# Kernel tuning notes

Hardware: AMD Instinct MI355X
Metric: run time of the kernel (lower is better)

Reference implementation:

```python
import jax, jax.numpy as jnp
import numpy as np

C_Z = 128
C_S = 1024
C_S_OUT = 1024
B, L = 1, 1024


def setup_inputs() -> dict:
    key = jax.random.key(0)
    ks = jax.random.split(key, 8)
    s_z = jax.random.normal(ks[0], (B, L, L, C_Z), dtype=jnp.float32)
    s_s_in = jax.random.normal(ks[1], (B, L, C_S), dtype=jnp.float32)
    pair_mask = jnp.ones((B, L, L), dtype=jnp.float32)
    scale = 0.02
    return {
        "s_z": s_z,
        "s_s_in": s_s_in,
        "pair_mask": pair_mask,
        "ln_g": jnp.ones((C_Z,), jnp.float32),
        "ln_b": jnp.zeros((C_Z,), jnp.float32),
        "w1": jax.random.normal(ks[2], (C_Z, C_Z), jnp.float32) * scale,
        "b1": jnp.zeros((C_Z,), jnp.float32),
        "w2": jax.random.normal(ks[3], (C_Z, C_Z), jnp.float32) * scale,
        "b2": jnp.zeros((C_Z,), jnp.float32),
        "wc": jax.random.normal(ks[4], (C_S_OUT, 2 * C_Z + C_S), jnp.float32) * scale,
        "bc": jnp.zeros((C_S_OUT,), jnp.float32),
    }


def _layernorm(x, g, b, eps=1e-5):
    mu = jnp.mean(x, axis=-1, keepdims=True)
    var = jnp.mean(jnp.square(x - mu), axis=-1, keepdims=True)
    return (x - mu) * jax.lax.rsqrt(var + eps) * g + b


def reference(s_z, s_s_in, pair_mask, ln_g, ln_b, w1, b1, w2, b2, wc, bc):
    # LayerNorm -> Linear -> ReLU -> Linear over last dim (c_z)
    z = _layernorm(s_z, ln_g, ln_b)
    z = jax.nn.relu(jnp.einsum("blmc,dc->blmd", z, w1) + b1)
    z = jnp.einsum("blmc,dc->blmd", z, w2) + b2
    z = z * pair_mask[..., None]
    # masked mean over columns (dim=2) and rows (dim=1)
    norm_c = jnp.clip(jnp.sum(pair_mask, axis=2), 1.0, None)  # (B, L)
    s_s_c = jnp.sum(z, axis=2) / norm_c[..., None]            # (B, L, c_z)
    norm_r = jnp.clip(jnp.sum(pair_mask, axis=1), 1.0, None)
    s_s_r = jnp.sum(z, axis=1) / norm_r[..., None]
    cat = jnp.concatenate([s_s_c, s_s_r, s_s_in], axis=-1)    # (B, L, 2*c_z + c_s)
    return jnp.einsum("blc,dc->bld", cat, wc) + bc            # (B, L, c_s_out)
```

## Files before the change

kernel.cpp:

```cpp
#include <hip/hip_runtime.h>
#include <hip/hip_bf16.h>


typedef short bf16x8 __attribute__((ext_vector_type(8)));
typedef float f32x16 __attribute__((ext_vector_type(16)));

static __device__ __forceinline__ short f2bf(float f) {
  unsigned u = __float_as_uint(f);
  u += 0x7fffu + ((u >> 16) & 1u);
  return (short)(u >> 16);
}
static __device__ __forceinline__ float bf2f(short s) {
  return __uint_as_float(((unsigned)(unsigned short)s) << 16);
}

__global__ __launch_bounds__(256, 2) void k_pair(
    const float* __restrict__ z, const float* __restrict__ pm,
    const float* __restrict__ lng, const float* __restrict__ lnb,
    const float* __restrict__ w1, const float* __restrict__ b1,
    float* __restrict__ g, float* __restrict__ gr)
{
  __shared__ __align__(16) char smemRaw[64 * 136 * 2];
  __shared__ float maskS[64];
  short* As   = (short*)smemRaw;
  float* red1 = (float*)smemRaw;

  const int tid  = threadIdx.x;
  const int lane = tid & 63;
  const int wv   = tid >> 6;
  const int rt   = wv >> 1;
  const int ch   = wv & 1;
  const int ln   = lane & 31;
  const int hh   = lane >> 5;
  const int l0   = blockIdx.y * 32;
  const int m0   = blockIdx.x * 32;
  const int c8   = (tid & 15) * 8;

  float lg[8], lb[8];
  #pragma unroll
  for (int j = 0; j < 8; ++j) { lg[j] = lng[c8 + j]; lb[j] = lnb[c8 + j]; }

  float b1v[2];
  #pragma unroll
  for (int cc = 0; cc < 2; ++cc) b1v[cc] = b1[(ch * 2 + cc) * 32 + ln];

  bf16x8 bF[2][8];
  #pragma unroll
  for (int cc = 0; cc < 2; ++cc) {
    const int n = (ch * 2 + cc) * 32 + ln;
    #pragma unroll
    for (int k0 = 0; k0 < 8; ++k0) {
      const float* wp = w1 + n * 128 + k0 * 16 + hh * 8;
      float4 f0 = *(const float4*)wp;
      float4 f1 = *(const float4*)(wp + 4);
      bf16x8 t;
      t[0]=f2bf(f0.x); t[1]=f2bf(f0.y); t[2]=f2bf(f0.z); t[3]=f2bf(f0.w);
      t[4]=f2bf(f1.x); t[5]=f2bf(f1.y); t[6]=f2bf(f1.z); t[7]=f2bf(f1.w);
      bF[cc][k0] = t;
    }
  }

  float grA[2][16];
  #pragma unroll
  for (int cc = 0; cc < 2; ++cc)
    #pragma unroll
    for (int i = 0; i < 16; ++i) grA[cc][i] = 0.f;

  #pragma unroll 1
  for (int b = 0; b < 16; ++b) {
    if (b) __syncthreads();
    float4 xa[4], xb[4];
    #pragma unroll
    for (int p = 0; p < 4; ++p) {
      const int r = p * 16 + (tid >> 4);
      const int l = l0 + b * 2 + (r >> 5);
      const int m = m0 + (r & 31);
      const float* src = z + ((size_t)l * 1024 + (size_t)m) * 128 + c8;
      xa[p] = *(const float4*)src;
      xb[p] = *(const float4*)(src + 4);
    }
    if (tid < 64) {
      const int l = l0 + b * 2 + (tid >> 5);
      maskS[tid] = pm[(size_t)l * 1024 + (m0 + (tid & 31))];
    }
    #pragma unroll
    for (int p = 0; p < 4; ++p) {
      const int r = p * 16 + (tid >> 4);
      float x[8] = {xa[p].x, xa[p].y, xa[p].z, xa[p].w,
                    xb[p].x, xb[p].y, xb[p].z, xb[p].w};
      float s = 0.f, s2 = 0.f;
      #pragma unroll
      for (int j = 0; j < 8; ++j) { s += x[j]; s2 += x[j] * x[j]; }
      #pragma unroll
      for (int off = 1; off < 16; off <<= 1) {
        s  += __shfl_xor(s, off);
        s2 += __shfl_xor(s2, off);
      }
      const float mu  = s * (1.f / 128.f);
      const float var = s2 * (1.f / 128.f) - mu * mu;
      const float rs  = rsqrtf(var + 1e-5f);
      bf16x8 o;
      #pragma unroll
      for (int j = 0; j < 8; ++j) o[j] = f2bf((x[j] - mu) * rs * lg[j] + lb[j]);
      *(bf16x8*)(As + r * 136 + c8) = o;
    }
    __syncthreads();

    f32x16 acc0, acc1;
    #pragma unroll
    for (int i = 0; i < 16; ++i) { acc0[i] = 0.f; acc1[i] = 0.f; }
    #pragma unroll
    for (int k0 = 0; k0 < 8; ++k0) {
      bf16x8 aF = *(bf16x8*)(As + (rt * 32 + ln) * 136 + k0 * 16 + hh * 8);
      acc0 = __builtin_amdgcn_mfma_f32_32x32x16_bf16(aF, bF[0][k0], acc0, 0, 0, 0);
      acc1 = __builtin_amdgcn_mfma_f32_32x32x16_bf16(aF, bF[1][k0], acc1, 0, 0, 0);
    }

    float mrow[16];
    #pragma unroll
    for (int i = 0; i < 16; ++i) {
      const int cr = (i & 3) + 8 * (i >> 2) + 4 * hh;
      mrow[i] = maskS[rt * 32 + cr];
    }
    const int lrow = l0 + b * 2 + rt;
    float s0 = 0.f, s1 = 0.f;
    #pragma unroll
    for (int i = 0; i < 16; ++i) {
      const float v0 = fmaxf(acc0[i] + b1v[0], 0.f) * mrow[i];
      const float v1 = fmaxf(acc1[i] + b1v[1], 0.f) * mrow[i];
      grA[0][i] += v0; grA[1][i] += v1;
      s0 += v0; s1 += v1;
    }
    s0 += __shfl_xor(s0, 32);
    s1 += __shfl_xor(s1, 32);
    if (lane < 32) {
      atomicAdd(&g[lrow * 128 + (ch * 2 + 0) * 32 + lane], s0);
      atomicAdd(&g[lrow * 128 + (ch * 2 + 1) * 32 + lane], s1);
    }
  }

  __syncthreads();
  if (rt == 1) {
    #pragma unroll
    for (int cc = 0; cc < 2; ++cc)
      #pragma unroll
      for (int i = 0; i < 16; ++i) {
        const int cr = (i & 3) + 8 * (i >> 2) + 4 * hh;
        red1[((ch * 2 + cc) * 32 + cr) * 32 + ln] = grA[cc][i];
      }
  }
  __syncthreads();
  if (rt == 0) {
    #pragma unroll
    for (int cc = 0; cc < 2; ++cc)
      #pragma unroll
      for (int i = 0; i < 16; ++i) {
        const int cr = (i & 3) + 8 * (i >> 2) + 4 * hh;
        const float v = grA[cc][i] + red1[((ch * 2 + cc) * 32 + cr) * 32 + ln];
        atomicAdd(&gr[(m0 + cr) * 128 + (ch * 2 + cc) * 32 + ln], v);
      }
  }
}

__global__ void k_masksum(const float* __restrict__ pm,
                          float* __restrict__ Mc, float* __restrict__ Mr)
{
  const int t = blockIdx.x * 256 + threadIdx.x;
  float s = 0.f;
  for (int l = 0; l < 1024; ++l) s += pm[(size_t)l * 1024 + t];
  Mr[t] = s;

  const int w = t >> 6, lane = t & 63;
  for (int l = w; l < 1024; l += 16) {
    float v = 0.f;
    #pragma unroll 4
    for (int i = 0; i < 16; ++i) v += pm[(size_t)l * 1024 + i * 64 + lane];
    #pragma unroll
    for (int off = 1; off < 64; off <<= 1) v += __shfl_xor(v, off);
    if (lane == 0) Mc[l] = v;
  }
}

__global__ __launch_bounds__(256, 2) void k_seqproj(
    const float* __restrict__ gg, const float* __restrict__ w2,
    const float* __restrict__ b2, const float* __restrict__ Mc,
    const float* __restrict__ Mr, float* __restrict__ ss)
{
  __shared__ __align__(16) char smemRaw[64 * 136 * 2];
  __shared__ float Mvs[64];
  short* As = (short*)smemRaw;

  const int tid = threadIdx.x, lane = tid & 63, wv = tid >> 6;
  const int rt = wv >> 1, ch = wv & 1, ln = lane & 31, hh = lane >> 5;
  const int r0 = blockIdx.x * 64;
  const int c8 = (tid & 15) * 8;

  float b2v[2];
  #pragma unroll
  for (int cc = 0; cc < 2; ++cc) b2v[cc] = b2[(ch * 2 + cc) * 32 + ln];

  bf16x8 bF[2][8];
  #pragma unroll
  for (int cc = 0; cc < 2; ++cc) {
    const int n = (ch * 2 + cc) * 32 + ln;
    #pragma unroll
    for (int k0 = 0; k0 < 8; ++k0) {
      const float* wp = w2 + n * 128 + k0 * 16 + hh * 8;
      float4 f0 = *(const float4*)wp;
      float4 f1 = *(const float4*)(wp + 4);
      bf16x8 t;
      t[0]=f2bf(f0.x); t[1]=f2bf(f0.y); t[2]=f2bf(f0.z); t[3]=f2bf(f0.w);
      t[4]=f2bf(f1.x); t[5]=f2bf(f1.y); t[6]=f2bf(f1.z); t[7]=f2bf(f1.w);
      bF[cc][k0] = t;
    }
  }

  #pragma unroll
  for (int p = 0; p < 4; ++p) {
    const int r = p * 16 + (tid >> 4);
    const float* src = gg + (size_t)(r0 + r) * 128 + c8;
    float4 f0 = *(const float4*)src;
    float4 f1 = *(const float4*)(src + 4);
    bf16x8 o;
    o[0]=f2bf(f0.x); o[1]=f2bf(f0.y); o[2]=f2bf(f0.z); o[3]=f2bf(f0.w);
    o[4]=f2bf(f1.x); o[5]=f2bf(f1.y); o[6]=f2bf(f1.z); o[7]=f2bf(f1.w);
    *(bf16x8*)(As + r * 136 + c8) = o;
  }
  if (tid < 64) {
    const int p = r0 + tid;
    Mvs[tid] = (p < 1024) ? Mc[p] : Mr[p - 1024];
  }
  __syncthreads();

  f32x16 acc0, acc1;
  #pragma unroll
  for (int i = 0; i < 16; ++i) { acc0[i] = 0.f; acc1[i] = 0.f; }
  #pragma unroll
  for (int k0 = 0; k0 < 8; ++k0) {
    bf16x8 aF = *(bf16x8*)(As + (rt * 32 + ln) * 136 + k0 * 16 + hh * 8);
    acc0 = __builtin_amdgcn_mfma_f32_32x32x16_bf16(aF, bF[0][k0], acc0, 0, 0, 0);
    acc1 = __builtin_amdgcn_mfma_f32_32x32x16_bf16(aF, bF[1][k0], acc1, 0, 0, 0);
  }

  #pragma unroll
  for (int i = 0; i < 16; ++i) {
    const int cr = (i & 3) + 8 * (i >> 2) + 4 * hh;
    const int p = r0 + rt * 32 + cr;
    const float mv = Mvs[rt * 32 + cr];
    const float dn = fmaxf(mv, 1.f);
    ss[(size_t)p * 128 + (ch * 2 + 0) * 32 + ln] = (acc0[i] + b2v[0] * mv) / dn;
    ss[(size_t)p * 128 + (ch * 2 + 1) * 32 + ln] = (acc1[i] + b2v[1] * mv) / dn;
  }
}

__global__ __launch_bounds__(256, 2) void k_final(
    const float* __restrict__ ss, const float* __restrict__ s_in,
    const float* __restrict__ wc, const float* __restrict__ bc,
    float* __restrict__ out)
{
  __shared__ __align__(16) short Ah[64 * 40], Al[64 * 40];
  __shared__ __align__(16) short Bh[64 * 40], Bl[64 * 40];
  const int tid = threadIdx.x, lane = tid & 63, wv = tid >> 6;
  const int mi = (wv >> 1) * 32, ni = (wv & 1) * 32;
  const int ln = lane & 31, hh = lane >> 5;
  const int m0 = blockIdx.y * 64, n0 = blockIdx.x * 64;
  const int rS = tid >> 2;
  const int kb = (tid & 3) * 8;

  const float bcv = bc[n0 + ni + ln];
  f32x16 acc;
  #pragma unroll
  for (int i = 0; i < 16; ++i) acc[i] = 0.f;

  #pragma unroll 1
  for (int kk0 = 0; kk0 < 1280; kk0 += 32) {
    if (kk0) __syncthreads();
    const float* srcA;
    if (kk0 < 128)      srcA = ss + (size_t)(m0 + rS) * 128 + kk0 + kb;
    else if (kk0 < 256) srcA = ss + (size_t)(1024 + m0 + rS) * 128 + (kk0 - 128) + kb;
    else                srcA = s_in + (size_t)(m0 + rS) * 1024 + (kk0 - 256) + kb;
    float4 a0 = *(const float4*)srcA;
    float4 a1 = *(const float4*)(srcA + 4);
    const float* srcB = wc + (size_t)(n0 + rS) * 1280 + kk0 + kb;
    float4 b0 = *(const float4*)srcB;
    float4 b1_ = *(const float4*)(srcB + 4);

    float av[8] = {a0.x,a0.y,a0.z,a0.w,a1.x,a1.y,a1.z,a1.w};
    float bv[8] = {b0.x,b0.y,b0.z,b0.w,b1_.x,b1_.y,b1_.z,b1_.w};
    bf16x8 vah, val_, vbh, vbl;
    #pragma unroll
    for (int j = 0; j < 8; ++j) {
      const short ha = f2bf(av[j]);
      vah[j] = ha; val_[j] = f2bf(av[j] - bf2f(ha));
      const short hb = f2bf(bv[j]);
      vbh[j] = hb; vbl[j] = f2bf(bv[j] - bf2f(hb));
    }
    *(bf16x8*)(Ah + rS * 40 + kb) = vah;
    *(bf16x8*)(Al + rS * 40 + kb) = val_;
    *(bf16x8*)(Bh + rS * 40 + kb) = vbh;
    *(bf16x8*)(Bl + rS * 40 + kb) = vbl;
    __syncthreads();

    #pragma unroll
    for (int k0 = 0; k0 < 2; ++k0) {
      bf16x8 aH = *(bf16x8*)(Ah + (mi + ln) * 40 + k0 * 16 + hh * 8);
      bf16x8 aL = *(bf16x8*)(Al + (mi + ln) * 40 + k0 * 16 + hh * 8);
      bf16x8 bH = *(bf16x8*)(Bh + (ni + ln) * 40 + k0 * 16 + hh * 8);
      bf16x8 bL = *(bf16x8*)(Bl + (ni + ln) * 40 + k0 * 16 + hh * 8);
      acc = __builtin_amdgcn_mfma_f32_32x32x16_bf16(aH, bH, acc, 0, 0, 0);
      acc = __builtin_amdgcn_mfma_f32_32x32x16_bf16(aH, bL, acc, 0, 0, 0);
      acc = __builtin_amdgcn_mfma_f32_32x32x16_bf16(aL, bH, acc, 0, 0, 0);
    }
  }

  #pragma unroll
  for (int i = 0; i < 16; ++i) {
    const int cr = (i & 3) + 8 * (i >> 2) + 4 * hh;
    out[(size_t)(m0 + mi + cr) * 1024 + n0 + ni + ln] = acc[i] + bcv;
  }
}

extern "C" void kernel_launch(void* const* d_in, const int* in_sizes, int n_in,
                              void* d_out, int out_size, void* d_ws, size_t ws_size,
                              hipStream_t stream) {
  const float* s_z    = (const float*)d_in[0];
  const float* s_s_in = (const float*)d_in[1];
  const float* pmask  = (const float*)d_in[2];
  const float* ln_g   = (const float*)d_in[3];
  const float* ln_b   = (const float*)d_in[4];
  const float* w1     = (const float*)d_in[5];
  const float* b1     = (const float*)d_in[6];
  const float* w2     = (const float*)d_in[7];
  const float* b2     = (const float*)d_in[8];
  const float* wc     = (const float*)d_in[9];
  const float* bc     = (const float*)d_in[10];
  float* outp = (float*)d_out;

  float* g  = (float*)d_ws;
  float* gr = g  + 1024 * 128;
  float* Mc = gr + 1024 * 128;
  float* Mr = Mc + 1024;
  float* ss = Mr + 1024;

  hipMemsetAsync(d_ws, 0, (size_t)2 * 1024 * 128 * sizeof(float), stream);

  k_pair<<<dim3(32, 32), 256, 0, stream>>>(s_z, pmask, ln_g, ln_b, w1, b1, g, gr);
  k_masksum<<<4, 256, 0, stream>>>(pmask, Mc, Mr);
  k_seqproj<<<32, 256, 0, stream>>>(g, w2, b2, Mc, Mr, ss);
  k_final<<<dim3(16, 16), 256, 0, stream>>>(ss, s_s_in, wc, bc, outp);
}
```

Measured before the change: 921.9 us.

## Double-buffer pair kernel, fuse mask sums, presplit final GEMM operands

The pair kernel now double-buffers its LDS tile and prefetches the next z rows into registers while the current MFMA runs. The separate masksum kernel is removed: row and column mask sums are accumulated inside k_pair with atomics. A new k_split kernel converts s_s_in and wc to bf16 hi/lo pairs ahead of time. k_seqproj writes its output directly as hi/lo bf16, so k_final only loads pre-split shorts, also with register prefetch. This adds an extra kernel and more workspace traffic, and doubles k_pair's LDS use, which may lower occupancy.

New measurement: 764.2 us. -17.1%, faster.

```diff
diff --git a/kernel.cpp b/kernel.cpp
--- a/kernel.cpp
+++ b/kernel.cpp
@@ -3,6 +3,7 @@
 
 
 typedef short bf16x8 __attribute__((ext_vector_type(8)));
+typedef short short4v __attribute__((ext_vector_type(4)));
 typedef float f32x16 __attribute__((ext_vector_type(16)));
 
 static __device__ __forceinline__ short f2bf(float f) {
@@ -18,12 +19,11 @@
     const float* __restrict__ z, const float* __restrict__ pm,
     const float* __restrict__ lng, const float* __restrict__ lnb,
     const float* __restrict__ w1, const float* __restrict__ b1,
-    float* __restrict__ g, float* __restrict__ gr)
+    float* __restrict__ g, float* __restrict__ gr,
+    float* __restrict__ Mc, float* __restrict__ Mr)
 {
-  __shared__ __align__(16) char smemRaw[64 * 136 * 2];
-  __shared__ float maskS[64];
-  short* As   = (short*)smemRaw;
-  float* red1 = (float*)smemRaw;
+  __shared__ __align__(16) short As[2][64 * 136];
+  __shared__ float maskS[2][64];
 
   const int tid  = threadIdx.x;
   const int lane = tid & 63;
@@ -65,11 +65,11 @@
   for (int cc = 0; cc < 2; ++cc)
     #pragma unroll
     for (int i = 0; i < 16; ++i) grA[cc][i] = 0.f;
-
-  #pragma unroll 1
-  for (int b = 0; b < 16; ++b) {
-    if (b) __syncthreads();
-    float4 xa[4], xb[4];
+  float mrAcc = 0.f;
+
+  float4 xa[4], xb[4];
+  float  mv = 0.f;
+  auto LOADB = [&](int b) {
     #pragma unroll
     for (int p = 0; p < 4; ++p) {
       const int r = p * 16 + (tid >> 4);
@@ -79,10 +79,15 @@
       xa[p] = *(const float4*)src;
       xb[p] = *(const float4*)(src + 4);
     }
-    if (tid < 64) {
-      const int l = l0 + b * 2 + (tid >> 5);
-      maskS[tid] = pm[(size_t)l * 1024 + (m0 + (tid & 31))];
-    }
+    if (tid < 64)
+      mv = pm[(size_t)(l0 + b * 2 + (tid >> 5)) * 1024 + (m0 + (tid & 31))];
+  };
+
+  LOADB(0);
+
+  #pragma unroll 1
+  for (int b = 0; b < 16; ++b) {
+    const int buf = b & 1;
     #pragma unroll
     for (int p = 0; p < 4; ++p) {
       const int r = p * 16 + (tid >> 4);
@@ -102,16 +107,19 @@
       bf16x8 o;
       #pragma unroll
       for (int j = 0; j < 8; ++j) o[j] = f2bf((x[j] - mu) * rs * lg[j] + lb[j]);
-      *(bf16x8*)(As + r * 136 + c8) = o;
-    }
+      *(bf16x8*)(&As[buf][r * 136 + c8]) = o;
+    }
+    if (tid < 64) maskS[buf][tid] = mv;
     __syncthreads();
 
+    if (b < 15) LOADB(b + 1);
+
     f32x16 acc0, acc1;
     #pragma unroll
     for (int i = 0; i < 16; ++i) { acc0[i] = 0.f; acc1[i] = 0.f; }
     #pragma unroll
     for (int k0 = 0; k0 < 8; ++k0) {
-      bf16x8 aF = *(bf16x8*)(As + (rt * 32 + ln) * 136 + k0 * 16 + hh * 8);
+      bf16x8 aF = *(bf16x8*)(&As[buf][(rt * 32 + ln) * 136 + k0 * 16 + hh * 8]);
       acc0 = __builtin_amdgcn_mfma_f32_32x32x16_bf16(aF, bF[0][k0], acc0, 0, 0, 0);
       acc1 = __builtin_amdgcn_mfma_f32_32x32x16_bf16(aF, bF[1][k0], acc1, 0, 0, 0);
     }
@@ -120,7 +128,7 @@
     #pragma unroll
     for (int i = 0; i < 16; ++i) {
       const int cr = (i & 3) + 8 * (i >> 2) + 4 * hh;
-      mrow[i] = maskS[rt * 32 + cr];
+      mrow[i] = maskS[buf][rt * 32 + cr];
     }
     const int lrow = l0 + b * 2 + rt;
     float s0 = 0.f, s1 = 0.f;
@@ -137,9 +145,24 @@
       atomicAdd(&g[lrow * 128 + (ch * 2 + 0) * 32 + lane], s0);
       atomicAdd(&g[lrow * 128 + (ch * 2 + 1) * 32 + lane], s1);
     }
+
+    if (wv == 0) {
+      const float v = maskS[buf][lane];
+      mrAcc += v;
+      float rsum = v;
+      #pragma unroll
+      for (int off = 1; off < 32; off <<= 1) rsum += __shfl_xor(rsum, off);
+      if (ln == 0) atomicAdd(&Mc[l0 + b * 2 + hh], rsum);
+    }
+  }
+
+  if (wv == 0) {
+    const float v = mrAcc + __shfl_xor(mrAcc, 32);
+    if (lane < 32) atomicAdd(&Mr[m0 + lane], v);
   }
 
   __syncthreads();
+  float* red1 = (float*)&As[0][0];
   if (rt == 1) {
     #pragma unroll
     for (int cc = 0; cc < 2; ++cc)
@@ -162,33 +185,13 @@
   }
 }
 
-__global__ void k_masksum(const float* __restrict__ pm,
-                          float* __restrict__ Mc, float* __restrict__ Mr)
-{
-  const int t = blockIdx.x * 256 + threadIdx.x;
-  float s = 0.f;
-  for (int l = 0; l < 1024; ++l) s += pm[(size_t)l * 1024 + t];
-  Mr[t] = s;
-
-  const int w = t >> 6, lane = t & 63;
-  for (int l = w; l < 1024; l += 16) {
-    float v = 0.f;
-    #pragma unroll 4
-    for (int i = 0; i < 16; ++i) v += pm[(size_t)l * 1024 + i * 64 + lane];
-    #pragma unroll
-    for (int off = 1; off < 64; off <<= 1) v += __shfl_xor(v, off);
-    if (lane == 0) Mc[l] = v;
-  }
-}
-
 __global__ __launch_bounds__(256, 2) void k_seqproj(
     const float* __restrict__ gg, const float* __restrict__ w2,
     const float* __restrict__ b2, const float* __restrict__ Mc,
-    const float* __restrict__ Mr, float* __restrict__ ss)
+    const float* __restrict__ Mr, short* __restrict__ Ah, short* __restrict__ Al)
 {
-  __shared__ __align__(16) char smemRaw[64 * 136 * 2];
+  __shared__ __align__(16) short As[64 * 136];
   __shared__ float Mvs[64];
-  short* As = (short*)smemRaw;
 
   const int tid = threadIdx.x, lane = tid & 63, wv = tid >> 6;
   const int rt = wv >> 1, ch = wv & 1, ln = lane & 31, hh = lane >> 5;
@@ -224,7 +227,7 @@
     bf16x8 o;
     o[0]=f2bf(f0.x); o[1]=f2bf(f0.y); o[2]=f2bf(f0.z); o[3]=f2bf(f0.w);
     o[4]=f2bf(f1.x); o[5]=f2bf(f1.y); o[6]=f2bf(f1.z); o[7]=f2bf(f1.w);
-    *(bf16x8*)(As + r * 136 + c8) = o;
+    *(bf16x8*)(&As[r * 136 + c8]) = o;
   }
   if (tid < 64) {
     const int p = r0 + tid;
@@ -237,29 +240,76 @@
   for (int i = 0; i < 16; ++i) { acc0[i] = 0.f; acc1[i] = 0.f; }
   #pragma unroll
   for (int k0 = 0; k0 < 8; ++k0) {
-    bf16x8 aF = *(bf16x8*)(As + (rt * 32 + ln) * 136 + k0 * 16 + hh * 8);
+    bf16x8 aF = *(bf16x8*)(&As[(rt * 32 + ln) * 136 + k0 * 16 + hh * 8]);
     acc0 = __builtin_amdgcn_mfma_f32_32x32x16_bf16(aF, bF[0][k0], acc0, 0, 0, 0);
     acc1 = __builtin_amdgcn_mfma_f32_32x32x16_bf16(aF, bF[1][k0], acc1, 0, 0, 0);
   }
 
+  const int base = (r0 < 1024) ? 0 : 128;
   #pragma unroll
   for (int i = 0; i < 16; ++i) {
     const int cr = (i & 3) + 8 * (i >> 2) + 4 * hh;
     const int p = r0 + rt * 32 + cr;
-    const float mv = Mvs[rt * 32 + cr];
-    const float dn = fmaxf(mv, 1.f);
-    ss[(size_t)p * 128 + (ch * 2 + 0) * 32 + ln] = (acc0[i] + b2v[0] * mv) / dn;
-    ss[(size_t)p * 128 + (ch * 2 + 1) * 32 + ln] = (acc1[i] + b2v[1] * mv) / dn;
+    const int row = p & 1023;
+    const float mvv = Mvs[rt * 32 + cr];
+    const float dn = fmaxf(mvv, 1.f);
+    const float v0 = (acc0[i] + b2v[0] * mvv) / dn;
+    const float v1 = (acc1[i] + b2v[1] * mvv) / dn;
+    const int c0 = base + (ch * 2 + 0) * 32 + ln;
+    const int c1 = base + (ch * 2 + 1) * 32 + ln;
+    const short h0 = f2bf(v0), h1 = f2bf(v1);
+    Ah[(size_t)row * 1280 + c0] = h0;
+    Al[(size_t)row * 1280 + c0] = f2bf(v0 - bf2f(h0));
+    Ah[(size_t)row * 1280 + c1] = h1;
+    Al[(size_t)row * 1280 + c1] = f2bf(v1 - bf2f(h1));
+  }
+}
+
+__global__ void k_split(const float* __restrict__ s_in, const float* __restrict__ wc,
+                        short* __restrict__ Ah, short* __restrict__ Al,
+                        short* __restrict__ Bh, short* __restrict__ Bl)
+{
+  const int idx = blockIdx.x * 256 + threadIdx.x;
+
+  if (idx < 262144) {
+    const int row = idx >> 8;
+    const int c4  = (idx & 255) * 4;
+    float4 v = *(const float4*)(s_in + (size_t)row * 1024 + c4);
+    float x[4] = {v.x, v.y, v.z, v.w};
+    short4v hi, lo;
+    #pragma unroll
+    for (int j = 0; j < 4; ++j) {
+      const short h = f2bf(x[j]);
+      hi[j] = h; lo[j] = f2bf(x[j] - bf2f(h));
+    }
+    const size_t o = (size_t)row * 1280 + 256 + c4;
+    *(short4v*)(Ah + o) = hi;
+    *(short4v*)(Al + o) = lo;
+  }
+  if (idx < 327680) {
+    const int row = idx / 320;
+    const int c4  = (idx - row * 320) * 4;
+    float4 v = *(const float4*)(wc + (size_t)row * 1280 + c4);
+    float x[4] = {v.x, v.y, v.z, v.w};
+    short4v hi, lo;
+    #pragma unroll
+    for (int j = 0; j < 4; ++j) {
+      const short h = f2bf(x[j]);
+      hi[j] = h; lo[j] = f2bf(x[j] - bf2f(h));
+    }
+    const size_t o = (size_t)row * 1280 + c4;
+    *(short4v*)(Bh + o) = hi;
+    *(short4v*)(Bl + o) = lo;
   }
 }
 
 __global__ __launch_bounds__(256, 2) void k_final(
-    const float* __restrict__ ss, const float* __restrict__ s_in,
-    const float* __restrict__ wc, const float* __restrict__ bc,
-    float* __restrict__ out)
+    const short* __restrict__ Ah, const short* __restrict__ Al,
+    const short* __restrict__ Bh, const short* __restrict__ Bl,
+    const float* __restrict__ bc, float* __restrict__ out)
 {
-  __shared__ __align__(16) short Ah[64 * 40], Al[64 * 40];
-  __shared__ __align__(16) short Bh[64 * 40], Bl[64 * 40];
+  __shared__ __align__(16) short sAh[64 * 40], sAl[64 * 40];
+  __shared__ __align__(16) short sBh[64 * 40], sBl[64 * 40];
   const int tid = threadIdx.x, lane = tid & 63, wv = tid >> 6;
   const int mi = (wv >> 1) * 32, ni = (wv & 1) * 32;
   const int ln = lane & 31, hh = lane >> 5;
@@ -272,41 +322,31 @@
   #pragma unroll
   for (int i = 0; i < 16; ++i) acc[i] = 0.f;
 
+  bf16x8 rAh, rAl, rBh, rBl;
+  auto LOADK = [&](int kk0) {
+    rAh = *(const bf16x8*)(Ah + (size_t)(m0 + rS) * 1280 + kk0 + kb);
+    rAl = *(const bf16x8*)(Al + (size_t)(m0 + rS) * 1280 + kk0 + kb);
+    rBh = *(const bf16x8*)(Bh + (size_t)(n0 + rS) * 1280 + kk0 + kb);
+    rBl = *(const bf16x8*)(Bl + (size_t)(n0 + rS) * 1280 + kk0 + kb);
+  };
+  LOADK(0);
+
   #pragma unroll 1
   for (int kk0 = 0; kk0 < 1280; kk0 += 32) {
     if (kk0) __syncthreads();
-    const float* srcA;
-    if (kk0 < 128)      srcA = ss + (size_t)(m0 + rS) * 128 + kk0 + kb;
-    else if (kk0 < 256) srcA = ss + (size_t)(1024 + m0 + rS) * 128 + (kk0 - 128) + kb;
-    else                srcA = s_in + (size_t)(m0 + rS) * 1024 + (kk0 - 256) + kb;
-    float4 a0 = *(const float4*)srcA;
-    float4 a1 = *(const float4*)(srcA + 4);
-    const float* srcB = wc + (size_t)(n0 + rS) * 1280 + kk0 + kb;
-    float4 b0 = *(const float4*)srcB;
-    float4 b1_ = *(const float4*)(srcB + 4);
-
-    float av[8] = {a0.x,a0.y,a0.z,a0.w,a1.x,a1.y,a1.z,a1.w};
-    float bv[8] = {b0.x,b0.y,b0.z,b0.w,b1_.x,b1_.y,b1_.z,b1_.w};
-    bf16x8 vah, val_, vbh, vbl;
-    #pragma unroll
-    for (int j = 0; j < 8; ++j) {
-      const short ha = f2bf(av[j]);
-      vah[j] = ha; val_[j] = f2bf(av[j] - bf2f(ha));
-      const short hb = f2bf(bv[j]);
-      vbh[j] = hb; vbl[j] = f2bf(bv[j] - bf2f(hb));
-    }
-    *(bf16x8*)(Ah + rS * 40 + kb) = vah;
-    *(bf16x8*)(Al + rS * 40 + kb) = val_;
-    *(bf16x8*)(Bh + rS * 40 + kb) = vbh;
-    *(bf16x8*)(Bl + rS * 40 + kb) = vbl;
+    *(bf16x8*)(sAh + rS * 40 + kb) = rAh;
+    *(bf16x8*)(sAl + rS * 40 + kb) = rAl;
+    *(bf16x8*)(sBh + rS * 40 + kb) = rBh;
+    *(bf16x8*)(sBl + rS * 40 + kb) = rBl;
     __syncthreads();
+    if (kk0 < 1280 - 32) LOADK(kk0 + 32);
 
     #pragma unroll
     for (int k0 = 0; k0 < 2; ++k0) {
-      bf16x8 aH = *(bf16x8*)(Ah + (mi + ln) * 40 + k0 * 16 + hh * 8);
-      bf16x8 aL = *(bf16x8*)(Al + (mi + ln) * 40 + k0 * 16 + hh * 8);
-      bf16x8 bH = *(bf16x8*)(Bh + (ni + ln) * 40 + k0 * 16 + hh * 8);
-      bf16x8 bL = *(bf16x8*)(Bl + (ni + ln) * 40 + k0 * 16 + hh * 8);
+      bf16x8 aH = *(bf16x8*)(sAh + (mi + ln) * 40 + k0 * 16 + hh * 8);
+      bf16x8 aL = *(bf16x8*)(sAl + (mi + ln) * 40 + k0 * 16 + hh * 8);
+      bf16x8 bH = *(bf16x8*)(sBh + (ni + ln) * 40 + k0 * 16 + hh * 8);
+      bf16x8 bL = *(bf16x8*)(sBl + (ni + ln) * 40 + k0 * 16 + hh * 8);
       acc = __builtin_amdgcn_mfma_f32_32x32x16_bf16(aH, bH, acc, 0, 0, 0);
       acc = __builtin_amdgcn_mfma_f32_32x32x16_bf16(aH, bL, acc, 0, 0, 0);
       acc = __builtin_amdgcn_mfma_f32_32x32x16_bf16(aL, bH, acc, 0, 0, 0);
@@ -340,12 +380,15 @@
   float* gr = g  + 1024 * 128;
   float* Mc = gr + 1024 * 128;
   float* Mr = Mc + 1024;
-  float* ss = Mr + 1024;
-
-  hipMemsetAsync(d_ws, 0, (size_t)2 * 1024 * 128 * sizeof(float), stream);
-
-  k_pair<<<dim3(32, 32), 256, 0, stream>>>(s_z, pmask, ln_g, ln_b, w1, b1, g, gr);
-  k_masksum<<<4, 256, 0, stream>>>(pmask, Mc, Mr);
-  k_seqproj<<<32, 256, 0, stream>>>(g, w2, b2, Mc, Mr, ss);
-  k_final<<<dim3(16, 16), 256, 0, stream>>>(ss, s_s_in, wc, bc, outp);
-}
+  short* Ah = (short*)(Mr + 1024);
+  short* Al = Ah + (size_t)1024 * 1280;
+  short* Bh = Al + (size_t)1024 * 1280;
+  short* Bl = Bh + (size_t)1024 * 1280;
+
+  hipMemsetAsync(d_ws, 0, (size_t)(2 * 1024 * 128 + 2048) * sizeof(float), stream);
+
+  k_split<<<1280, 256, 0, stream>>>(s_s_in, wc, Ah, Al, Bh, Bl);
+  k_pair<<<dim3(32, 32), 256, 0, stream>>>(s_z, pmask, ln_g, ln_b, w1, b1, g, gr, Mc, Mr);
+  k_seqproj<<<32, 256, 0, stream>>>(g, w2, b2, Mc, Mr, Ah, Al);
+  k_final<<<dim3(16, 16), 256, 0, stream>>>(Ah, Al, Bh, Bl, bc, outp);
+}
```
